# Optimization experiments

Measured on AMD Instinct MI355X. Metric: run time of the kernel, lower is better.

## Reference

```python
import jax, jax.numpy as jnp
import numpy as np

NUM_FEAT = 64        # per-head dim == input channel C
HIDDEN = 1024        # total hidden size
NUM_HEADS = HIDDEN // NUM_FEAT  # 16


def setup_inputs() -> dict:
    key = jax.random.key(0)
    k1, k2, k3, k4, k5 = jax.random.split(key, 5)
    B, N, C = 4, 2048, NUM_FEAT
    hidden_states = jax.random.normal(k1, (B, N, C), dtype=jnp.float32)
    # nn.Linear(num_feat, hidden*3): weight [3*hidden, num_feat], store transposed for x @ W
    s_qkv = 1.0 / np.sqrt(C)
    qkv_w = jax.random.uniform(k2, (C, 3 * HIDDEN), jnp.float32, -s_qkv, s_qkv)
    qkv_b = jax.random.uniform(k3, (3 * HIDDEN,), jnp.float32, -s_qkv, s_qkv)
    s_out = 1.0 / np.sqrt(HIDDEN)
    out_w = jax.random.uniform(k4, (HIDDEN, C), jnp.float32, -s_out, s_out)
    out_b = jax.random.uniform(k5, (C,), jnp.float32, -s_out, s_out)
    return {"hidden_states": hidden_states, "qkv_w": qkv_w, "qkv_b": qkv_b,
            "out_w": out_w, "out_b": out_b}


def reference(hidden_states, qkv_w, qkv_b, out_w, out_b):
    B, N, C = hidden_states.shape
    H, D = NUM_HEADS, NUM_FEAT  # head count, head dim
    # qkv projection: [B,N,3*HIDDEN] -> [3,B,H,N,D]
    qkv = hidden_states @ qkv_w + qkv_b
    qkv = qkv.reshape(B, N, 3, H, D).transpose(2, 0, 3, 1, 4)
    q, k, v = qkv[0], qkv[1], qkv[2]
    # scaled dot-product attention with materialized scores (faithful to source)
    scores = jnp.einsum('bhqd,bhkd->bhqk', q, k) / jnp.sqrt(jnp.float32(D))
    probs = jax.nn.softmax(scores, axis=-1)
    ctx = jnp.einsum('bhqk,bhkd->bhqd', probs, v)           # [B,H,N,D]
    ctx = ctx.transpose(0, 2, 1, 3).reshape(B, N, H * D)    # [B,N,HIDDEN]
    out = ctx @ out_w + out_b                               # [B,N,C]
    return jax.nn.gelu(out, approximate=False)
```

## Files before the change

kernel.cpp:

```cpp
#include <hip/hip_runtime.h>
#include <math.h>

#define B_ 4
#define N_ 2048
#define C_ 64
#define H_ 16
#define D_ 64
#define HID 1024

#define QSCALE 0.18033688011112042f

typedef short bf16x8 __attribute__((ext_vector_type(8)));
typedef unsigned short u16x8 __attribute__((ext_vector_type(8)));
typedef float f32x4 __attribute__((ext_vector_type(4)));

#define MFMA(a, b, c) __builtin_amdgcn_mfma_f32_16x16x32_bf16((a), (b), (c), 0, 0, 0)

typedef __attribute__((address_space(3))) void lds_t;
typedef const __attribute__((address_space(1))) void gbl_t;
#define ASYNC16(g, l) __builtin_amdgcn_global_load_lds((gbl_t*)(g), (lds_t*)(l), 16, 0, 0)

static __device__ __forceinline__ unsigned short f2bf(float f) {
  unsigned u = __float_as_uint(f);
  u += 0x7FFFu + ((u >> 16) & 1u);
  return (unsigned short)(u >> 16);
}
static __device__ __forceinline__ float bf2f(unsigned short h) {
  return __uint_as_float((unsigned)h << 16);
}
static __device__ __forceinline__ unsigned pkbf(float a, float b) {
  return __builtin_amdgcn_perm(__float_as_uint(b), __float_as_uint(a),
                               0x07060302u);
}

__global__ __launch_bounds__(256, 2) void qkv_kernel(
    const float* __restrict__ X, const float* __restrict__ W,
    const float* __restrict__ bias, const float* __restrict__ W2,
    unsigned short* __restrict__ Qhi, unsigned short* __restrict__ Khi,
    unsigned short* __restrict__ Vhi,
    unsigned short* __restrict__ W2THi, unsigned short* __restrict__ W2TLo) {
  const int t = threadIdx.x;
  const int ct = blockIdx.x;
  const int tt = blockIdx.y;

  if (ct == 24) {
    int idx0 = tt * 1024 + t * 4;
#pragma unroll
    for (int e = 0; e < 4; ++e) {
      int idx = idx0 + e;
      int k = idx & 1023, col = idx >> 10;
      float v = W2[(size_t)k * 64 + col];
      unsigned short hi = f2bf(v);
      W2THi[(size_t)col * 1024 + k] = hi;
      W2TLo[(size_t)col * 1024 + k] = f2bf(v - bf2f(hi));
    }
    return;
  }

  __shared__ float Xl[128][68];
  __shared__ float Wl[64][132];

#pragma unroll
  for (int i = 0; i < 8; ++i) {
    int idx = t + 256 * i;
    int tok = idx >> 4, f4 = (idx & 15) * 4;
    *(f32x4*)&Xl[tok][f4] =
        *(const f32x4*)&X[(size_t)(tt * 128 + tok) * 64 + f4];
  }
#pragma unroll
  for (int i = 0; i < 8; ++i) {
    int idx = t + 256 * i;
    int c = idx >> 5, f4 = (idx & 31) * 4;
    *(f32x4*)&Wl[c][f4] = *(const f32x4*)&W[(size_t)c * 3072 + ct * 128 + f4];
  }
  __syncthreads();

  const int tokg = t >> 4;
  const int colg = t & 15;
  float acc[8][8];
#pragma unroll
  for (int i = 0; i < 8; ++i)
#pragma unroll
    for (int c = 0; c < 8; ++c) acc[i][c] = 0.f;

  for (int c4 = 0; c4 < 64; c4 += 4) {
    f32x4 wr[4][2];
#pragma unroll
    for (int j = 0; j < 4; ++j) {
      wr[j][0] = *(const f32x4*)&Wl[c4 + j][colg * 8];
      wr[j][1] = *(const f32x4*)&Wl[c4 + j][colg * 8 + 4];
    }
#pragma unroll
    for (int i = 0; i < 8; ++i) {
      f32x4 x = *(const f32x4*)&Xl[tokg * 8 + i][c4];
#pragma unroll
      for (int j = 0; j < 4; ++j)
#pragma unroll
        for (int cc = 0; cc < 4; ++cc) {
          acc[i][cc] += x[j] * wr[j][0][cc];
          acc[i][cc + 4] += x[j] * wr[j][1][cc];
        }
    }
  }

  const int s = ct >> 3;
  const float scale = (s == 0) ? QSCALE : 1.0f;
  const int col0 = ct * 128 + colg * 8;
  const int hh = (col0 >> 6) & 15, d0 = col0 & 63;
  float bia[8];
#pragma unroll
  for (int cc = 0; cc < 8; ++cc) bia[cc] = bias[col0 + cc];
#pragma unroll
  for (int i = 0; i < 8; ++i)
#pragma unroll
    for (int cc = 0; cc < 8; ++cc) acc[i][cc] = (acc[i][cc] + bia[cc]) * scale;

  if (s == 2) {
    __syncthreads();
    unsigned(*sT)[65] = (unsigned(*)[65])Xl;
#pragma unroll
    for (int cc = 0; cc < 8; ++cc)
#pragma unroll
      for (int pr = 0; pr < 4; ++pr) {
        unsigned h2 = (unsigned)f2bf(acc[pr * 2][cc]) |
                      ((unsigned)f2bf(acc[pr * 2 + 1][cc]) << 16);
        sT[colg * 8 + cc][tokg * 4 + pr] = h2;
      }
    __syncthreads();
    const int col = t >> 1, half = t & 1;
    const int hvb = (ct & 7) * 2;
    const int bbv = tt >> 4;
    const int n0 = (tt & 15) * 128 + half * 64;
    size_t row = (size_t)((bbv * H_ + hvb + (col >> 6)) * D_ + (col & 63));
    unsigned short* dst = Vhi + row * (size_t)N_ + n0;
#pragma unroll
    for (int k = 0; k < 8; ++k)
      *(uint4*)(dst + k * 8) = *(const uint4*)&sT[col][half * 32 + k * 4];
  } else {
    unsigned short* A = (s == 0) ? Qhi : Khi;
    const int bb = (tt * 128) >> 11;
#pragma unroll
    for (int i = 0; i < 8; ++i) {
      int token = tt * 128 + tokg * 8 + i;
      int n = token & 2047;
      size_t dst = ((size_t)(bb * H_ + hh) * N_ + n) * D_ + d0;
      u16x8 h8;
#pragma unroll
      for (int cc = 0; cc < 8; ++cc) h8[cc] = f2bf(acc[i][cc]);
      *(u16x8*)&A[dst] = h8;
    }
  }
}

__global__ __launch_bounds__(256, 4) void attn_kernel(
    const unsigned short* __restrict__ Qhi, const unsigned short* __restrict__ Khi,
    const unsigned short* __restrict__ VThi,
    unsigned short* __restrict__ ctxHi, unsigned short* __restrict__ ctxLo) {
  __shared__ unsigned short smem[12288];

  const int tid = threadIdx.x;
  const int w = tid >> 6, lane = tid & 63;
  const int lid = lane & 15, quad = lane >> 4;
  const int l7 = lid & 7;
  unsigned short* sK = smem;
  unsigned short* sVt = smem + 4096;
  unsigned short* sP = smem + 8192 + w * 1024;

  const int id = blockIdx.x;
  const int bh = id & 63;
  const int qt = id >> 6;
  const int b = bh >> 4, h = bh & 15;
  const size_t base = (size_t)bh * N_ * D_;
  const int row0 = qt * 128 + w * 32;

  bf16x8 qh[2][2];
#pragma unroll
  for (int mt = 0; mt < 2; ++mt) {
    int row = row0 + mt * 16 + lid;
    const unsigned short* qph = Qhi + base + (size_t)row * D_;
#pragma unroll
    for (int kc = 0; kc < 2; ++kc)
      qh[mt][kc] = *(const bf16x8*)(qph + kc * 32 + quad * 8);
  }

  f32x4 o[2][4];
  float lacc[2] = {0.f, 0.f};
#pragma unroll
  for (int mt = 0; mt < 2; ++mt)
#pragma unroll
    for (int dnt = 0; dnt < 4; ++dnt) o[mt][dnt] = (f32x4){0.f, 0.f, 0.f, 0.f};

  const int lrow = lane >> 3;
  const int lgr = (lane & 7) ^ lrow;

  auto stage = [&](int kt_, int buf_) {
    size_t gk = base + (size_t)(kt_ * 32 + w * 8 + lrow) * 64 + lgr * 8;
    ASYNC16(Khi + gk, sK + buf_ * 2048 + (w * 8) * 64);
    int pr = w * 8 + lrow;
    int vd = pr * 2 + (lgr >> 2);
    int vk0 = (lgr & 3) * 8;
    size_t gv = base + (size_t)vd * N_ + kt_ * 32 + vk0;
    ASYNC16(VThi + gv, sVt + buf_ * 2048 + (w * 8) * 64);
  };

  stage(0, 0);

  for (int kt = 0; kt < N_ / 32; ++kt) {
    const int buf = kt & 1;
    __syncthreads();
    if (kt + 1 < N_ / 32) stage(kt + 1, buf ^ 1);

    f32x4 sc[2][2];
#pragma unroll
    for (int nt = 0; nt < 2; ++nt) {
      int key = nt * 16 + lid;
#pragma unroll
      for (int kc = 0; kc < 2; ++kc) {
        int off = key * 64 + (((kc * 4 + quad) ^ l7) << 3);
        bf16x8 kh_ = *(const bf16x8*)&sK[buf * 2048 + off];
#pragma unroll
        for (int mt = 0; mt < 2; ++mt) {
          f32x4 c = (kc == 0) ? (f32x4){0.f, 0.f, 0.f, 0.f} : sc[mt][nt];
          c = MFMA(kh_, qh[mt][kc], c);
          sc[mt][nt] = c;
        }
      }
    }

    bf16x8 pa[2];
#pragma unroll
    for (int mt = 0; mt < 2; ++mt) {
      float lsum = 0.f;
#pragma unroll
      for (int nt = 0; nt < 2; ++nt) {
        float p0 = __builtin_amdgcn_exp2f(sc[mt][nt][0]);
        float p1 = __builtin_amdgcn_exp2f(sc[mt][nt][1]);
        float p2 = __builtin_amdgcn_exp2f(sc[mt][nt][2]);
        float p3 = __builtin_amdgcn_exp2f(sc[mt][nt][3]);
        lsum += (p0 + p1) + (p2 + p3);
        uint2 dw;
        dw.x = pkbf(p0, p1);
        dw.y = pkbf(p2, p3);
        int idx = (mt * 8 + (lid >> 1)) * 64 +
                  (((nt * 2 + (quad >> 1) + 4 * (lid & 1)) ^ ((lid >> 1) & 7))
                   << 3) +
                  (quad & 1) * 4;
        *(uint2*)&sP[idx] = dw;
      }
      lsum += __shfl_xor(lsum, 16);
      lsum += __shfl_xor(lsum, 32);
      lacc[mt] += lsum;
      int ridx = (mt * 8 + (lid >> 1)) * 64 +
                 (((quad + 4 * (lid & 1)) ^ ((lid >> 1) & 7)) << 3);
      pa[mt] = *(const bf16x8*)&sP[ridx];
    }

#pragma unroll
    for (int dnt = 0; dnt < 4; ++dnt) {
      int voff = buf * 2048 + (dnt * 8 + (lid >> 1)) * 64 +
                 (((quad + (lid & 1) * 4) ^ ((lid >> 1) & 7)) << 3);
      bf16x8 vh = *(const bf16x8*)&sVt[voff];
#pragma unroll
      for (int mt = 0; mt < 2; ++mt) o[mt][dnt] = MFMA(vh, pa[mt], o[mt][dnt]);
    }
  }

  __syncthreads();
  float* scr = (float*)smem + w * 1088;
  const int erow = lane >> 2, ecq = lane & 3;
#pragma unroll
  for (int mt = 0; mt < 2; ++mt) {
    float inv = 1.0f / lacc[mt];
#pragma unroll
    for (int dnt = 0; dnt < 4; ++dnt) {
      f32x4 v = o[mt][dnt] * inv;
      *(f32x4*)&scr[lid * 68 + dnt * 16 + quad * 4] = v;
    }
    int token = b * N_ + row0 + mt * 16 + erow;
    size_t doff = (size_t)token * HID + h * 64;
#pragma unroll
    for (int i = 0; i < 4; ++i) {
      f32x4 v4 = *(const f32x4*)&scr[erow * 68 + ecq * 4 + i * 16];
      unsigned short hi_[4], lo_[4];
#pragma unroll
      for (int j = 0; j < 4; ++j) {
        hi_[j] = f2bf(v4[j]);
        lo_[j] = f2bf(v4[j] - bf2f(hi_[j]));
      }
      uint2 hw, lw;
      hw.x = (unsigned)hi_[0] | ((unsigned)hi_[1] << 16);
      hw.y = (unsigned)hi_[2] | ((unsigned)hi_[3] << 16);
      lw.x = (unsigned)lo_[0] | ((unsigned)lo_[1] << 16);
      lw.y = (unsigned)lo_[2] | ((unsigned)lo_[3] << 16);
      *(uint2*)&ctxHi[doff + ecq * 4 + i * 16] = hw;
      *(uint2*)&ctxLo[doff + ecq * 4 + i * 16] = lw;
    }
  }
}

__global__ __launch_bounds__(256) void out_kernel(
    const unsigned short* __restrict__ ctxHi, const unsigned short* __restrict__ ctxLo,
    const unsigned short* __restrict__ W2THi, const unsigned short* __restrict__ W2TLo,
    const float* __restrict__ b2, float* __restrict__ out) {
  __shared__ float sO[2][2][4][16][16];
  const int tid = threadIdx.x;
  const int w = tid >> 6, lane = tid & 63;
  const int pair = w >> 1, kh = w & 1;
  const int lid = lane & 15, quad = lane >> 4;
  const int tok0 = blockIdx.x * 32 + pair * 16;

  f32x4 acc[4];
#pragma unroll
  for (int nt = 0; nt < 4; ++nt) acc[nt] = (f32x4){0.f, 0.f, 0.f, 0.f};

  const size_t abase = (size_t)(tok0 + lid) * HID + kh * 512 + quad * 8;

  for (int kc = 0; kc < 16; ++kc) {
    bf16x8 ah = *(const bf16x8*)&ctxHi[abase + kc * 32];
    bf16x8 al = *(const bf16x8*)&ctxLo[abase + kc * 32];
#pragma unroll
    for (int nt = 0; nt < 4; ++nt) {
      size_t boff =
          (size_t)(nt * 16 + lid) * HID + kh * 512 + kc * 32 + quad * 8;
      bf16x8 bh = *(const bf16x8*)&W2THi[boff];
      bf16x8 bl = *(const bf16x8*)&W2TLo[boff];
      f32x4 c = acc[nt];
      c = MFMA(ah, bh, c);
      c = MFMA(ah, bl, c);
      c = MFMA(al, bh, c);
      acc[nt] = c;
    }
  }

#pragma unroll
  for (int nt = 0; nt < 4; ++nt)
#pragma unroll
    for (int r = 0; r < 4; ++r) sO[pair][kh][nt][quad * 4 + r][lid] = acc[nt][r];
  __syncthreads();
  if (kh == 0) {
#pragma unroll
    for (int nt = 0; nt < 4; ++nt)
#pragma unroll
      for (int r = 0; r < 4; ++r) {
        int token = tok0 + quad * 4 + r;
        int col = nt * 16 + lid;
        float v = sO[pair][0][nt][quad * 4 + r][lid] +
                  sO[pair][1][nt][quad * 4 + r][lid] + b2[col];
        float g = 0.5f * v * (1.0f + erff(v * 0.70710678118654752f));
        out[(size_t)token * 64 + col] = g;
      }
  }
}

extern "C" void kernel_launch(void* const* d_in, const int* in_sizes, int n_in,
                              void* d_out, int out_size, void* d_ws, size_t ws_size,
                              hipStream_t stream) {
  const float* X = (const float*)d_in[0];
  const float* qkv_w = (const float*)d_in[1];
  const float* qkv_b = (const float*)d_in[2];
  const float* out_w = (const float*)d_in[3];
  const float* out_b = (const float*)d_in[4];
  float* out = (float*)d_out;

  const size_t NE = (size_t)B_ * H_ * N_ * D_;
  unsigned short* ws16 = (unsigned short*)d_ws;
  unsigned short* Qhi = ws16 + 0 * NE;
  unsigned short* Khi = ws16 + 1 * NE;
  unsigned short* VThi = ws16 + 2 * NE;
  unsigned short* ctxHi = ws16 + 3 * NE;
  unsigned short* ctxLo = ws16 + 4 * NE;
  unsigned short* W2THi = ws16 + 5 * NE;
  unsigned short* W2TLo = W2THi + 65536;

  qkv_kernel<<<dim3(25, 64), 256, 0, stream>>>(X, qkv_w, qkv_b, out_w, Qhi,
                                               Khi, VThi, W2THi, W2TLo);
  attn_kernel<<<1024, 256, 0, stream>>>(Qhi, Khi, VThi, ctxHi, ctxLo);
  out_kernel<<<256, 256, 0, stream>>>(ctxHi, ctxLo, W2THi, W2TLo, out_b, out);
}
```

Measured before the change: 216.6 us.

## Use split-bf16 MFMA for QKV projection instead of FP32 FMA loops

```diff
diff --git a/kernel.cpp b/kernel.cpp
--- a/kernel.cpp
+++ b/kernel.cpp
@@ -57,98 +57,151 @@
     return;
   }
 
-  __shared__ float Xl[128][68];
-  __shared__ float Wl[64][132];
-
-#pragma unroll
-  for (int i = 0; i < 8; ++i) {
-    int idx = t + 256 * i;
-    int tok = idx >> 4, f4 = (idx & 15) * 4;
-    *(f32x4*)&Xl[tok][f4] =
-        *(const f32x4*)&X[(size_t)(tt * 128 + tok) * 64 + f4];
-  }
-#pragma unroll
-  for (int i = 0; i < 8; ++i) {
-    int idx = t + 256 * i;
-    int c = idx >> 5, f4 = (idx & 31) * 4;
-    *(f32x4*)&Wl[c][f4] = *(const f32x4*)&W[(size_t)c * 3072 + ct * 128 + f4];
+  __shared__ unsigned short qsmem[32768];
+  unsigned short* sXhi = qsmem;
+  unsigned short* sXlo = qsmem + 8192;
+  unsigned short* sWhi = qsmem + 16384;
+  unsigned short* sWlo = qsmem + 24576;
+
+  {
+    const int kg = t & 7, r0 = t >> 3;
+#pragma unroll
+    for (int i = 0; i < 4; ++i) {
+      int row = r0 + i * 32;
+      const float* src = &X[(size_t)(tt * 128 + row) * 64 + kg * 8];
+      f32x4 a = *(const f32x4*)src;
+      f32x4 b = *(const f32x4*)(src + 4);
+      u16x8 hi8, lo8;
+#pragma unroll
+      for (int j = 0; j < 4; ++j) {
+        hi8[j] = f2bf(a[j]);
+        lo8[j] = f2bf(a[j] - bf2f(hi8[j]));
+        hi8[4 + j] = f2bf(b[j]);
+        lo8[4 + j] = f2bf(b[j] - bf2f(hi8[4 + j]));
+      }
+      int off = row * 64 + ((kg ^ (row & 7)) << 3);
+      *(u16x8*)&sXhi[off] = hi8;
+      *(u16x8*)&sXlo[off] = lo8;
+    }
+  }
+  {
+    const int col = t & 127, kg0 = t >> 7;
+#pragma unroll
+    for (int i = 0; i < 4; ++i) {
+      int kg = kg0 + i * 2;
+      u16x8 hi8, lo8;
+#pragma unroll
+      for (int j = 0; j < 8; ++j) {
+        float v = W[(size_t)(kg * 8 + j) * 3072 + ct * 128 + col];
+        unsigned short h = f2bf(v);
+        hi8[j] = h;
+        lo8[j] = f2bf(v - bf2f(h));
+      }
+      int off = col * 64 + ((kg ^ (col & 7)) << 3);
+      *(u16x8*)&sWhi[off] = hi8;
+      *(u16x8*)&sWlo[off] = lo8;
+    }
   }
   __syncthreads();
 
-  const int tokg = t >> 4;
-  const int colg = t & 15;
-  float acc[8][8];
-#pragma unroll
-  for (int i = 0; i < 8; ++i)
-#pragma unroll
-    for (int c = 0; c < 8; ++c) acc[i][c] = 0.f;
-
-  for (int c4 = 0; c4 < 64; c4 += 4) {
-    f32x4 wr[4][2];
-#pragma unroll
-    for (int j = 0; j < 4; ++j) {
-      wr[j][0] = *(const f32x4*)&Wl[c4 + j][colg * 8];
-      wr[j][1] = *(const f32x4*)&Wl[c4 + j][colg * 8 + 4];
-    }
-#pragma unroll
-    for (int i = 0; i < 8; ++i) {
-      f32x4 x = *(const f32x4*)&Xl[tokg * 8 + i][c4];
-#pragma unroll
-      for (int j = 0; j < 4; ++j)
-#pragma unroll
-        for (int cc = 0; cc < 4; ++cc) {
-          acc[i][cc] += x[j] * wr[j][0][cc];
-          acc[i][cc + 4] += x[j] * wr[j][1][cc];
-        }
-    }
-  }
+  const int w = t >> 6, lane = t & 63;
+  const int lid = lane & 15, quad = lane >> 4;
+
+  bf16x8 xa[2][2][2];
+#pragma unroll
+  for (int mt = 0; mt < 2; ++mt) {
+    int row = w * 32 + mt * 16 + lid;
+#pragma unroll
+    for (int kc = 0; kc < 2; ++kc) {
+      int off = row * 64 + (((kc * 4 + quad) ^ (row & 7)) << 3);
+      xa[mt][kc][0] = *(const bf16x8*)&sXhi[off];
+      xa[mt][kc][1] = *(const bf16x8*)&sXlo[off];
+    }
+  }
+
+  f32x4 acc[2][8];
+#pragma unroll
+  for (int mt = 0; mt < 2; ++mt)
+#pragma unroll
+    for (int nt = 0; nt < 8; ++nt) acc[mt][nt] = (f32x4){0.f, 0.f, 0.f, 0.f};
+
+#pragma unroll
+  for (int nt = 0; nt < 8; ++nt) {
+    int col = nt * 16 + lid;
+#pragma unroll
+    for (int kc = 0; kc < 2; ++kc) {
+      int boff = col * 64 + (((kc * 4 + quad) ^ (col & 7)) << 3);
+      bf16x8 wbh = *(const bf16x8*)&sWhi[boff];
+      bf16x8 wbl = *(const bf16x8*)&sWlo[boff];
+#pragma unroll
+      for (int mt = 0; mt < 2; ++mt) {
+        f32x4 c = acc[mt][nt];
+        c = MFMA(xa[mt][kc][0], wbh, c);
+        c = MFMA(xa[mt][kc][0], wbl, c);
+        c = MFMA(xa[mt][kc][1], wbh, c);
+        acc[mt][nt] = c;
+      }
+    }
+  }
+
+  __syncthreads();
 
   const int s = ct >> 3;
   const float scale = (s == 0) ? QSCALE : 1.0f;
-  const int col0 = ct * 128 + colg * 8;
-  const int hh = (col0 >> 6) & 15, d0 = col0 & 63;
-  float bia[8];
-#pragma unroll
-  for (int cc = 0; cc < 8; ++cc) bia[cc] = bias[col0 + cc];
-#pragma unroll
-  for (int i = 0; i < 8; ++i)
-#pragma unroll
-    for (int cc = 0; cc < 8; ++cc) acc[i][cc] = (acc[i][cc] + bia[cc]) * scale;
-
-  if (s == 2) {
+  float bias_r[8];
+#pragma unroll
+  for (int nt = 0; nt < 8; ++nt) bias_r[nt] = bias[ct * 128 + nt * 16 + lid];
+
+  if (s < 2) {
+    unsigned short(*sOut)[136] = (unsigned short(*)[136])qsmem;
+#pragma unroll
+    for (int mt = 0; mt < 2; ++mt)
+#pragma unroll
+      for (int nt = 0; nt < 8; ++nt) {
+        f32x4 v = acc[mt][nt];
+#pragma unroll
+        for (int r = 0; r < 4; ++r)
+          sOut[w * 32 + mt * 16 + quad * 4 + r][nt * 16 + lid] =
+              f2bf((v[r] + bias_r[nt]) * scale);
+      }
     __syncthreads();
-    unsigned(*sT)[65] = (unsigned(*)[65])Xl;
-#pragma unroll
-    for (int cc = 0; cc < 8; ++cc)
-#pragma unroll
-      for (int pr = 0; pr < 4; ++pr) {
-        unsigned h2 = (unsigned)f2bf(acc[pr * 2][cc]) |
-                      ((unsigned)f2bf(acc[pr * 2 + 1][cc]) << 16);
-        sT[colg * 8 + cc][tokg * 4 + pr] = h2;
+    const int ltok = t >> 1, half = t & 1;
+    const int token = tt * 128 + ltok;
+    const int bb = token >> 11, n = token & 2047;
+    const int head = (ct * 2 + half) & 15;
+    unsigned short* A = (s == 0) ? Qhi : Khi;
+    size_t dst = ((size_t)(bb * H_ + head) * N_ + n) * D_;
+    const unsigned short* srcr = &sOut[ltok][half * 64];
+#pragma unroll
+    for (int j = 0; j < 8; ++j)
+      *(uint4*)&A[dst + j * 8] = *(const uint4*)&srcr[j * 8];
+  } else {
+    unsigned short(*sT)[136] = (unsigned short(*)[136])qsmem;
+#pragma unroll
+    for (int mt = 0; mt < 2; ++mt)
+#pragma unroll
+      for (int nt = 0; nt < 8; ++nt) {
+        f32x4 v = acc[mt][nt];
+        unsigned short h0 = f2bf(v[0] + bias_r[nt]);
+        unsigned short h1 = f2bf(v[1] + bias_r[nt]);
+        unsigned short h2 = f2bf(v[2] + bias_r[nt]);
+        unsigned short h3 = f2bf(v[3] + bias_r[nt]);
+        uint2 dw;
+        dw.x = (unsigned)h0 | ((unsigned)h1 << 16);
+        dw.y = (unsigned)h2 | ((unsigned)h3 << 16);
+        *(uint2*)&sT[nt * 16 + lid][w * 32 + mt * 16 + quad * 4] = dw;
       }
     __syncthreads();
     const int col = t >> 1, half = t & 1;
-    const int hvb = (ct & 7) * 2;
+    const int hv = (ct & 7) * 2 + (col >> 6), d = col & 63;
     const int bbv = tt >> 4;
     const int n0 = (tt & 15) * 128 + half * 64;
-    size_t row = (size_t)((bbv * H_ + hvb + (col >> 6)) * D_ + (col & 63));
-    unsigned short* dst = Vhi + row * (size_t)N_ + n0;
-#pragma unroll
-    for (int k = 0; k < 8; ++k)
-      *(uint4*)(dst + k * 8) = *(const uint4*)&sT[col][half * 32 + k * 4];
-  } else {
-    unsigned short* A = (s == 0) ? Qhi : Khi;
-    const int bb = (tt * 128) >> 11;
-#pragma unroll
-    for (int i = 0; i < 8; ++i) {
-      int token = tt * 128 + tokg * 8 + i;
-      int n = token & 2047;
-      size_t dst = ((size_t)(bb * H_ + hh) * N_ + n) * D_ + d0;
-      u16x8 h8;
-#pragma unroll
-      for (int cc = 0; cc < 8; ++cc) h8[cc] = f2bf(acc[i][cc]);
-      *(u16x8*)&A[dst] = h8;
-    }
+    size_t row = (size_t)((bbv * H_ + hv) * D_ + d);
+    unsigned short* dstp = Vhi + row * (size_t)N_ + n0;
+    const unsigned short* srcr = &sT[col][half * 64];
+#pragma unroll
+    for (int j = 0; j < 8; ++j)
+      *(uint4*)(dstp + j * 8) = *(const uint4*)&srcr[j * 8];
   }
 }
 
```

Result: faster. 206.5 us (-4.6%).
